# Kernel tuning notes

Hardware: AMD Instinct MI355X
Metric: run time of the kernel (lower is better)

The kernel has to match this reference:

```python
import jax, jax.numpy as jnp
import numpy as np

T, B, X, H, Y, D = 512, 64, 64, 1024, 64, 2


def setup_inputs() -> dict:
    key = jax.random.key(0)
    ks = jax.random.split(key, 13)
    s = 0.02  # weight init scale
    return {
        "x": jax.random.normal(ks[0], (T, B, X), dtype=jnp.float32),
        "enc_w": jax.random.normal(ks[1], (H, X), dtype=jnp.float32) * s,
        "enc_b": jax.random.normal(ks[2], (H,), dtype=jnp.float32) * s,
        "w_ih": jax.random.normal(ks[3], (D, 3 * H, H), dtype=jnp.float32) * s,
        "w_hh": jax.random.normal(ks[4], (D, 3 * H, H), dtype=jnp.float32) * s,
        "b_ih": jax.random.normal(ks[5], (D, 3 * H), dtype=jnp.float32) * s,
        "b_hh": jax.random.normal(ks[6], (D, 3 * H), dtype=jnp.float32) * s,
        "dec_w": jax.random.normal(ks[7], (H, H), dtype=jnp.float32) * s,
        "dec_b": jax.random.normal(ks[8], (H,), dtype=jnp.float32) * s,
        "exp_w": jax.random.normal(ks[9], (Y, H), dtype=jnp.float32) * s,
        "exp_b": jax.random.normal(ks[10], (Y,), dtype=jnp.float32) * s,
        "log_w": jax.random.normal(ks[11], (Y, H), dtype=jnp.float32) * s,
        "log_b": jax.random.normal(ks[12], (Y,), dtype=jnp.float32) * s,
    }


def _gru_cell(x, h, wih, whh, bih, bhh):
    # PyTorch GRUCell semantics
    gi = x @ wih.T + bih  # [B, 3H]
    gh = h @ whh.T + bhh  # [B, 3H]
    i_r, i_z, i_n = jnp.split(gi, 3, axis=-1)
    h_r, h_z, h_n = jnp.split(gh, 3, axis=-1)
    r = jax.nn.sigmoid(i_r + h_r)
    z = jax.nn.sigmoid(i_z + h_z)
    n = jnp.tanh(i_n + r * h_n)
    return (1.0 - z) * n + z * h


def reference(x, enc_w, enc_b, w_ih, w_hh, b_ih, b_hh, dec_w, dec_b,
              exp_w, exp_b, log_w, log_b):
    depth = w_ih.shape[0]
    batch = x.shape[1]
    h0 = jnp.zeros((depth, batch, w_hh.shape[-1]), dtype=x.dtype)

    def step(h_states, x_t):
        rnn_in = jnp.tanh(x_t @ enc_w.T + enc_b)  # encoder
        new_h = []
        for i in range(depth):  # small fixed stack of structurally distinct cells
            h = _gru_cell(rnn_in, h_states[i], w_ih[i], w_hh[i], b_ih[i], b_hh[i])
            new_h.append(h)
            rnn_in = h
        rnn_out = jnp.tanh(rnn_in @ dec_w.T + dec_b)  # decoder
        mean = rnn_out @ exp_w.T + exp_b
        var = jnp.exp(rnn_out @ log_w.T + log_b)
        return jnp.stack(new_h), (mean, var)

    _, (time_mean, time_var) = jax.lax.scan(step, h0, x)
    return time_mean, time_var  # each [T, B, Y]
```

## Files before the change

### kernel.cpp

```cpp
#include <hip/hip_runtime.h>
#include <hip/hip_bf16.h>
#include <cstdint>

#define T_STEPS 512
#define BATCH   64
#define XDIM    64
#define HDIM    1024
#define YDIM    64
#define BH      (BATCH * HDIM)
#define RING_D  32

#define WBLK_BYTES   98304
#define COMBO_BYTES  24576
#define TL1_OFF      16384

typedef unsigned short ushort_t;
typedef uint32_t u32;
typedef unsigned long long u64;
typedef __attribute__((ext_vector_type(8))) short short8;
typedef __attribute__((ext_vector_type(4))) float f32x4;

union U4S8 { uint4 u; short8 s; };

__device__ __forceinline__ u32 f2bf_u(float x) {
  u32 u = __float_as_uint(x);
  return (u + 0x7fffu + ((u >> 16) & 1u)) >> 16;
}
__device__ __forceinline__ ushort_t f2bf(float x) { return (ushort_t)f2bf_u(x); }

__device__ __forceinline__ float sigm(float x) { return 1.0f / (1.0f + expf(-x)); }

__device__ __forceinline__ void st_sc32(u32* p, u32 v) {
  __hip_atomic_store(p, v, __ATOMIC_RELAXED, __HIP_MEMORY_SCOPE_AGENT);
}

__device__ __forceinline__ uint4 ld_g128(const ushort_t* p) {
  uint4 r;
  asm volatile("global_load_dwordx4 %0, %1, off" : "=v"(r) : "v"(p));
  return r;
}

__device__ __forceinline__ int flags_ok(const u32* p, u32 tag) {
  uint4 f;
  asm volatile("global_load_dwordx4 %0, %1, off sc1\n\ts_waitcnt vmcnt(0)"
               : "=v"(f) : "v"(p) : "memory");
  return (f.x >= tag) && (f.y >= tag) && (f.z >= tag) && (f.w >= tag);
}
__device__ __forceinline__ void poll4(const u32* flags, int t, u32 tag) {
  const u32* p = flags + 4 * t;
  while (!flags_ok(p, tag)) __builtin_amdgcn_s_sleep(1);
}

__global__ __launch_bounds__(256) void enc_kernel(
    const float* __restrict__ x, const float* __restrict__ enc_w,
    const float* __restrict__ enc_b, ushort_t* __restrict__ enc_out)
{
  __shared__ float wlds[64 * 65];
  const int lane = threadIdx.x & 63;
  const int wv   = threadIdx.x >> 6;
  const int cb = blockIdx.x & 15;
  const int rb = blockIdx.x >> 4;
  const int j  = cb * 64 + lane;
  const int r0 = rb * 16 + wv * 4;

  const float* wsrc = enc_w + (size_t)cb * 64 * XDIM;
  for (int i = threadIdx.x; i < 4096; i += 256)
    wlds[(i >> 6) * 65 + (i & 63)] = wsrc[i];
  __syncthreads();

  const float* xr = x + (size_t)r0 * XDIM;
  float acc[4] = {0.f, 0.f, 0.f, 0.f};
#pragma unroll
  for (int k = 0; k < XDIM; k += 4) {
    const float w0 = wlds[lane * 65 + k];
    const float w1 = wlds[lane * 65 + k + 1];
    const float w2 = wlds[lane * 65 + k + 2];
    const float w3 = wlds[lane * 65 + k + 3];
#pragma unroll
    for (int rr = 0; rr < 4; ++rr) {
      const float* xp = xr + rr * XDIM + k;
      acc[rr] = fmaf(xp[3], w3, fmaf(xp[2], w2, fmaf(xp[1], w1, fmaf(xp[0], w0, acc[rr]))));
    }
  }
  const float b = enc_b[j];
#pragma unroll
  for (int rr = 0; rr < 4; ++rr)
    enc_out[(size_t)(r0 + rr) * HDIM + j] = f2bf(tanhf(acc[rr] + b));
}

__global__ __launch_bounds__(256) void wprep_kernel(
    const float* __restrict__ w_ih, const float* __restrict__ w_hh,
    ushort_t* __restrict__ wfrag)
{
  const int lane = threadIdx.x & 63;
  const int wv   = threadIdx.x >> 6;
  const int c    = blockIdx.x * 4 + wv;
  const int ko = c & 15;
  const int tl = (c >> 4) & 1;
  const int c2 = (c >> 5) & 3;
  const int bid = c >> 7;
  const int g = c2 >> 1, kh = c2 & 1;
  const int layer = bid >> 7;
  const int j0 = (bid & 127) * 8;
  const float* wsrc = (g ? w_hh : w_ih) + (size_t)layer * 3 * HDIM * HDIM;

  if (tl == 0) {
    const int col = lane & 15, kgrp = lane >> 4;
    const int k = kh * 512 + ko * 32 + kgrp * 8;
    const int row = (col < 8) ? (j0 + col) : (HDIM + j0 + col - 8);
    const float* src = wsrc + (size_t)row * HDIM + k;
    short8 v;
#pragma unroll
    for (int e = 0; e < 8; ++e) v[e] = (short)f2bf(src[e]);
    const size_t byte = (size_t)bid * WBLK_BYTES + c2 * COMBO_BYTES + ko * 1024 + lane * 16;
    *(short8*)((char*)wfrag + byte) = v;
  } else if (lane < 32) {
    const int kgrp = lane >> 3, col = lane & 7;
    const int k = kh * 512 + ko * 32 + kgrp * 8;
    const int row = 2 * HDIM + j0 + col;
    const float* src = wsrc + (size_t)row * HDIM + k;
    short8 v;
#pragma unroll
    for (int e = 0; e < 8; ++e) v[e] = (short)f2bf(src[e]);
    const size_t byte = (size_t)bid * WBLK_BYTES + c2 * COMBO_BYTES + TL1_OFF + ko * 512 + lane * 16;
    *(short8*)((char*)wfrag + byte) = v;
  }
}

__global__ __launch_bounds__(256) void wprep2_kernel(
    const float* __restrict__ dec_w, const float* __restrict__ exp_w,
    const float* __restrict__ log_w,
    ushort_t* __restrict__ dwfrag, ushort_t* __restrict__ hwfrag)
{
  const int lane = threadIdx.x & 63;
  const int wv   = threadIdx.x >> 6;
  const int c    = blockIdx.x * 4 + wv;
  short8 v;
  if (c < 2048) {
    const int nt = c >> 5, kc = c & 31;
    const int row = nt * 16 + (lane & 15);
    const int k   = kc * 32 + (lane >> 4) * 8;
    const float* src = dec_w + (size_t)row * HDIM + k;
#pragma unroll
    for (int e = 0; e < 8; ++e) v[e] = (short)f2bf(src[e]);
    *(short8*)(dwfrag + (size_t)c * 512 + lane * 8) = v;
  } else {
    const int c2 = c - 2048;
    const int nt = c2 >> 5, kc = c2 & 31;
    const int row = nt * 16 + (lane & 15);
    const int k   = kc * 32 + (lane >> 4) * 8;
    const float* src = (row < 64) ? (exp_w + (size_t)row * HDIM + k)
                                  : (log_w + (size_t)(row - 64) * HDIM + k);
#pragma unroll
    for (int e = 0; e < 8; ++e) v[e] = (short)f2bf(src[e]);
    *(short8*)(hwfrag + (size_t)c2 * 512 + lane * 8) = v;
  }
}

__global__ __launch_bounds__(512, 1) void rnn_persist(
    const ushort_t* __restrict__ ench1,
    const ushort_t* __restrict__ wfrag,
    const float* __restrict__ b_ih, const float* __restrict__ b_hh,
    ushort_t* __restrict__ h0ring,
    ushort_t* __restrict__ h1ring,
    ushort_t* __restrict__ h1_all,
    u32* __restrict__ l0_flags, u32* __restrict__ l1_flags)
{
  extern __shared__ char smem[];
  float* lds_part = (float*)(smem + WBLK_BYTES);

  const int tid  = threadIdx.x;
  const int lane = tid & 63;
  const int wid  = tid >> 6;
  const int bid  = blockIdx.x;
  const int layer = bid >> 7;
  const int j0    = (bid & 127) * 8;
  const int mp = wid & 1, g = (wid >> 1) & 1, kh = wid >> 2;
  const int col = lane & 15, kgrp = lane >> 4;
  const bool isL1 = (layer == 1);
  const int gbid = bid & 127;
  u32* ownf = isL1 ? l1_flags : l0_flags;

  {
    const uint4* src = (const uint4*)((const char*)wfrag + (size_t)bid * WBLK_BYTES);
    uint4* dst = (uint4*)smem;
#pragma unroll 4
    for (int i = tid; i < WBLK_BYTES / 16; i += 512) dst[i] = src[i];
  }

  const int c2 = g * 2 + kh;
  const char* w0 = smem + c2 * COMBO_BYTES + lane * 16;
  const char* w1 = smem + c2 * COMBO_BYTES + TL1_OFF + (kgrp * 8 + (col & 7)) * 16;

  float bA = 0.f, bB = 0.f, bC = 0.f;
  {
    const float* bi = b_ih + layer * 3 * HDIM;
    const float* bh = b_hh + layer * 3 * HDIM;
    if (col < 8) {
      const int j = j0 + col;
      bA = bi[j] + bh[j];
      bB = bi[2 * HDIM + j];
      bC = bh[2 * HDIM + j];
    } else {
      const int j = j0 + col - 8;
      bA = bi[HDIM + j] + bh[HDIM + j];
    }
  }

  f32x4 hp = {0.f, 0.f, 0.f, 0.f};

  __syncthreads();

  for (int i = 0; i < T_STEPS; ++i) {
    if (isL1) {
      if (tid < 32) poll4(l0_flags, tid, (u32)(i + 1));
      __syncthreads();
    }

    const ushort_t* A1 = isL1 ? (h0ring + (size_t)(i & (RING_D - 1)) * BH)
                              : (ench1 + (size_t)i * BH);
    const ushort_t* A2 = isL1 ? (h1ring + (size_t)((i - 1) & (RING_D - 1)) * BH)
                              : (h0ring + (size_t)((i - 1) & (RING_D - 1)) * BH);
    const ushort_t* A = g ? A2 : A1;
    const ushort_t* Arow0 = A + (size_t)(mp * 32 + col) * HDIM + kh * 512 + kgrp * 8;
    const ushort_t* Arow1 = Arow0 + 16 * HDIM;

    uint4 areg[32];
    if (g == 0) {
#pragma unroll
      for (int ko = 0; ko < 16; ++ko) {
        areg[2 * ko]     = ld_g128(Arow0 + ko * 32);
        areg[2 * ko + 1] = ld_g128(Arow1 + ko * 32);
      }
    }

    if (tid < 32) {
      poll4(ownf, tid, (u32)i);
      if (!isL1 && i >= RING_D) poll4(l1_flags, tid, (u32)(i - RING_D + 1));
    }
    __syncthreads();

    if (g == 1) {
#pragma unroll
      for (int ko = 0; ko < 16; ++ko) {
        areg[2 * ko]     = ld_g128(Arow0 + ko * 32);
        areg[2 * ko + 1] = ld_g128(Arow1 + ko * 32);
      }
    }

    f32x4 acc00 = {0,0,0,0}, acc01 = {0,0,0,0}, acc10 = {0,0,0,0}, acc11 = {0,0,0,0};
    asm volatile("s_waitcnt vmcnt(16)" ::: "memory");
    __builtin_amdgcn_sched_barrier(0);
#pragma unroll
    for (int ko = 0; ko < 8; ++ko) {
      const short8 b0 = *(const short8*)(w0 + ko * 1024);
      const short8 b1 = *(const short8*)(w1 + ko * 512);
      U4S8 a0, a1; a0.u = areg[2 * ko]; a1.u = areg[2 * ko + 1];
      acc00 = __builtin_amdgcn_mfma_f32_16x16x32_bf16(a0.s, b0, acc00, 0, 0, 0);
      acc01 = __builtin_amdgcn_mfma_f32_16x16x32_bf16(a0.s, b1, acc01, 0, 0, 0);
      acc10 = __builtin_amdgcn_mfma_f32_16x16x32_bf16(a1.s, b0, acc10, 0, 0, 0);
      acc11 = __builtin_amdgcn_mfma_f32_16x16x32_bf16(a1.s, b1, acc11, 0, 0, 0);
    }
    asm volatile("s_waitcnt vmcnt(0)" ::: "memory");
    __builtin_amdgcn_sched_barrier(0);
#pragma unroll
    for (int ko = 8; ko < 16; ++ko) {
      const short8 b0 = *(const short8*)(w0 + ko * 1024);
      const short8 b1 = *(const short8*)(w1 + ko * 512);
      U4S8 a0, a1; a0.u = areg[2 * ko]; a1.u = areg[2 * ko + 1];
      acc00 = __builtin_amdgcn_mfma_f32_16x16x32_bf16(a0.s, b0, acc00, 0, 0, 0);
      acc01 = __builtin_amdgcn_mfma_f32_16x16x32_bf16(a0.s, b1, acc01, 0, 0, 0);
      acc10 = __builtin_amdgcn_mfma_f32_16x16x32_bf16(a1.s, b0, acc10, 0, 0, 0);
      acc11 = __builtin_amdgcn_mfma_f32_16x16x32_bf16(a1.s, b1, acc11, 0, 0, 0);
    }

    const int base = (wid * 4) * 256 + lane * 4;
    *(f32x4*)&lds_part[base      ] = acc00;
    *(f32x4*)&lds_part[base + 256] = acc01;
    *(f32x4*)&lds_part[base + 512] = acc10;
    *(f32x4*)&lds_part[base + 768] = acc11;

    __syncthreads();

    if (wid < 4) {
      const int m = wid, mpe = m >> 1, ime = m & 1;
      const int i00 = ((0 * 4 + 0 * 2 + mpe) * 4 + ime * 2);
      const int i01 = ((1 * 4 + 0 * 2 + mpe) * 4 + ime * 2);
      const int i10 = ((0 * 4 + 1 * 2 + mpe) * 4 + ime * 2);
      const int i11 = ((1 * 4 + 1 * 2 + mpe) * 4 + ime * 2);
      const int lo = lane * 4;
      f32x4 girz = *(f32x4*)&lds_part[i00 * 256 + lo] + *(f32x4*)&lds_part[i01 * 256 + lo];
      f32x4 gin  = *(f32x4*)&lds_part[(i00 + 1) * 256 + lo] + *(f32x4*)&lds_part[(i01 + 1) * 256 + lo];
      f32x4 ghrz = *(f32x4*)&lds_part[i10 * 256 + lo] + *(f32x4*)&lds_part[i11 * 256 + lo];
      f32x4 ghn  = *(f32x4*)&lds_part[(i10 + 1) * 256 + lo] + *(f32x4*)&lds_part[(i11 + 1) * 256 + lo];

      ushort_t* hdst = isL1 ? (h1ring + (size_t)(i & (RING_D - 1)) * BH)
                            : (h0ring + (size_t)(i & (RING_D - 1)) * BH);
      ushort_t* hall = isL1 ? (h1_all + (size_t)i * BH) : (ushort_t*)0;

#pragma unroll
      for (int e = 0; e < 4; ++e) {
        const float rz = sigm(girz[e] + ghrz[e] + bA);
        const float nv = tanhf(gin[e] + bB + rz * (ghn[e] + bC));
        const float zv = __shfl_xor(rz, 8);
        const int b = m * 16 + kgrp * 4 + e;
        float h = 0.f;
        if (col < 8) {
          h = (1.f - zv) * nv + zv * hp[e];
          hp[e] = h;
        }
        const u32 hb = f2bf_u(h);
        const u32 pb = (u32)__shfl_xor((int)hb, 1);
        if (col < 8 && (col & 1) == 0) {
          const u32 pack = hb | (pb << 16);
          st_sc32((u32*)(hdst + b * HDIM + j0 + col), pack);
          if (hall) st_sc32((u32*)(hall + b * HDIM + j0 + col), pack);
        }
      }
    }

    __syncthreads();
    if (tid == 0) st_sc32(ownf + gbid, (u32)(i + 1));
  }
}

#define AST 1032
__global__ __launch_bounds__(512, 1) void dechead_kernel(
    const ushort_t* __restrict__ h1_all,
    const ushort_t* __restrict__ dwfrag, const ushort_t* __restrict__ hwfrag,
    const float* __restrict__ dec_b, const float* __restrict__ exp_b,
    const float* __restrict__ log_b, float* __restrict__ out)
{
  extern __shared__ char smem2[];
  ushort_t* Alds = (ushort_t*)smem2;
  ushort_t* Rlds = Alds + 32 * AST;

  const int tid  = threadIdx.x;
  const int lane = tid & 63;
  const int wv   = tid >> 6;
  const int base = blockIdx.x * 32;

  {
    const uint4* src = (const uint4*)(h1_all + (size_t)base * HDIM);
#pragma unroll
    for (int ii = 0; ii < 8; ++ii) {
      const int idx = ii * 512 + tid;
      const int row = idx >> 7;
      const int k   = (idx & 127) * 8;
      *(uint4*)(Alds + row * AST + k) = src[idx];
    }
  }
  __syncthreads();

  f32x4 acc[8][2];
#pragma unroll
  for (int t = 0; t < 8; ++t) { acc[t][0] = (f32x4){0,0,0,0}; acc[t][1] = (f32x4){0,0,0,0}; }

  const int r0 = lane & 15, kg = lane >> 4;
  const int nt0 = wv * 8;
#pragma unroll 1
  for (int t = 0; t < 8; ++t) {
    const ushort_t* bsrc = dwfrag + (size_t)(nt0 + t) * 32 * 512 + lane * 8;
    f32x4 c0 = acc[t][0], c1 = acc[t][1];
#pragma unroll
    for (int kc = 0; kc < 32; ++kc) {
      const short8 b  = *(const short8*)(bsrc + kc * 512);
      const short8 a0 = *(const short8*)(Alds + r0 * AST + kc * 32 + kg * 8);
      const short8 a1 = *(const short8*)(Alds + (16 + r0) * AST + kc * 32 + kg * 8);
      c0 = __builtin_amdgcn_mfma_f32_16x16x32_bf16(a0, b, c0, 0, 0, 0);
      c1 = __builtin_amdgcn_mfma_f32_16x16x32_bf16(a1, b, c1, 0, 0, 0);
    }
    acc[t][0] = c0; acc[t][1] = c1;
  }

#pragma unroll
  for (int t = 0; t < 8; ++t) {
    const int colc = (nt0 + t) * 16 + r0;
    const float db = dec_b[colc];
#pragma unroll
    for (int m = 0; m < 2; ++m) {
      const f32x4 v = acc[t][m];
#pragma unroll
      for (int e = 0; e < 4; ++e) {
        const int row = m * 16 + kg * 4 + e;
        Rlds[row * AST + colc] = (ushort_t)f2bf_u(tanhf(v[e] + db));
      }
    }
  }
  __syncthreads();

  f32x4 h0a = {0,0,0,0}, h1a = {0,0,0,0};
  {
    const ushort_t* bsrc = hwfrag + (size_t)wv * 32 * 512 + lane * 8;
#pragma unroll
    for (int kc = 0; kc < 32; ++kc) {
      const short8 b  = *(const short8*)(bsrc + kc * 512);
      const short8 a0 = *(const short8*)(Rlds + r0 * AST + kc * 32 + kg * 8);
      const short8 a1 = *(const short8*)(Rlds + (16 + r0) * AST + kc * 32 + kg * 8);
      h0a = __builtin_amdgcn_mfma_f32_16x16x32_bf16(a0, b, h0a, 0, 0, 0);
      h1a = __builtin_amdgcn_mfma_f32_16x16x32_bf16(a1, b, h1a, 0, 0, 0);
    }
  }
  const int y = wv * 16 + r0;
  if (wv < 4) {
    const float eb = exp_b[y];
#pragma unroll
    for (int m = 0; m < 2; ++m) {
      const f32x4 v = (m == 0) ? h0a : h1a;
#pragma unroll
      for (int e = 0; e < 4; ++e) {
        const int row = m * 16 + kg * 4 + e;
        out[(size_t)(base + row) * YDIM + y] = v[e] + eb;
      }
    }
  } else {
    const int yv = y - 64;
    const float lb = log_b[yv];
#pragma unroll
    for (int m = 0; m < 2; ++m) {
      const f32x4 v = (m == 0) ? h0a : h1a;
#pragma unroll
      for (int e = 0; e < 4; ++e) {
        const int row = m * 16 + kg * 4 + e;
        out[(size_t)(T_STEPS * BATCH * YDIM) + (size_t)(base + row) * YDIM + yv] = expf(v[e] + lb);
      }
    }
  }
}

extern "C" void kernel_launch(void* const* d_in, const int* in_sizes, int n_in,
                              void* d_out, int out_size, void* d_ws, size_t ws_size,
                              hipStream_t stream) {
  (void)in_sizes; (void)n_in; (void)out_size; (void)ws_size;
  const float* x     = (const float*)d_in[0];
  const float* enc_w = (const float*)d_in[1];
  const float* enc_b = (const float*)d_in[2];
  const float* w_ih  = (const float*)d_in[3];
  const float* w_hh  = (const float*)d_in[4];
  const float* b_ih  = (const float*)d_in[5];
  const float* b_hh  = (const float*)d_in[6];
  const float* dec_w = (const float*)d_in[7];
  const float* dec_b = (const float*)d_in[8];
  const float* exp_w = (const float*)d_in[9];
  const float* exp_b = (const float*)d_in[10];
  const float* log_w = (const float*)d_in[11];
  const float* log_b = (const float*)d_in[12];
  float* out = (float*)d_out;

  char* ws = (char*)d_ws;
  u32*      l0f     = (u32*)ws;
  u32*      l1f     = (u32*)(ws + 4096);
  ushort_t* wfrag   = (ushort_t*)(ws + 2097152);
  ushort_t* h0ring  = (ushort_t*)(ws + 27262976);
  ushort_t* h1ring  = (ushort_t*)(ws + 31457280);
  ushort_t* ench1   = (ushort_t*)(ws + 35651584);
  ushort_t* dwfrag  = (ushort_t*)(ws + 102760448);
  ushort_t* hwfrag  = (ushort_t*)(ws + 104857600);

  hipMemsetAsync(ws, 0, 8192, stream);
  hipMemsetAsync(ws + 27262976, 0, 8388608, stream);

  enc_kernel<<<32768, 256, 0, stream>>>(x, enc_w, enc_b, ench1);
  wprep_kernel<<<8192, 256, 0, stream>>>(w_ih, w_hh, wfrag);
  wprep2_kernel<<<576, 256, 0, stream>>>(dec_w, exp_w, log_w, dwfrag, hwfrag);

  {
    static int lds_opted = 0;
    if (!lds_opted) {
      hipFuncSetAttribute((const void*)rnn_persist,
                          hipFuncAttributeMaxDynamicSharedMemorySize, 131072);
      hipFuncSetAttribute((const void*)dechead_kernel,
                          hipFuncAttributeMaxDynamicSharedMemorySize, 2 * 32 * AST * 2);
      lds_opted = 1;
    }
    void* args[9];
    args[0] = (void*)&ench1;
    args[1] = (void*)&wfrag;
    args[2] = (void*)&b_ih;
    args[3] = (void*)&b_hh;
    args[4] = (void*)&h0ring;
    args[5] = (void*)&h1ring;
    args[6] = (void*)&ench1;
    args[7] = (void*)&l0f;
    args[8] = (void*)&l1f;
    hipLaunchCooperativeKernel((const void*)rnn_persist, dim3(256), dim3(512),
                               args, 131072, stream);
  }

  dechead_kernel<<<1024, 512, 2 * 32 * AST * 2, stream>>>(
      ench1, dwfrag, hwfrag, dec_b, exp_b, log_b, out);
}
```

Baseline: 5.573 ms.

## Per-wave flag polling on padded flags and coalesced 128-bit hidden-state stores

Replaces the block-wide poll-then-__syncthreads handshake with per-lane polling: each wave spins on its own dependency flags, which are now padded to one per 64-byte line. This lets waves start their global loads independently instead of waiting on a block barrier. Hidden-state outputs are staged in LDS and written as 128-bit row stores instead of scattered 32-bit atomic stores. The trade-off is many more lanes polling global memory each step and a slightly larger LDS footprint.

```diff
diff --git a/kernel.cpp b/kernel.cpp
--- a/kernel.cpp
+++ b/kernel.cpp
@@ -13,6 +13,7 @@
 #define WBLK_BYTES   98304
 #define COMBO_BYTES  24576
 #define TL1_OFF      16384
+#define LDS_TOTAL    (WBLK_BYTES + 32768 + 1024)
 
 typedef unsigned short ushort_t;
 typedef uint32_t u32;
@@ -33,22 +34,21 @@
 __device__ __forceinline__ void st_sc32(u32* p, u32 v) {
   __hip_atomic_store(p, v, __ATOMIC_RELAXED, __HIP_MEMORY_SCOPE_AGENT);
 }
-
+__device__ __forceinline__ void poll_lane(const u32* flags, int idx, u32 tag) {
+  const u32* p = flags + (size_t)idx * 16;
+  while (__hip_atomic_load((u32*)p, __ATOMIC_RELAXED, __HIP_MEMORY_SCOPE_AGENT) < tag)
+    __builtin_amdgcn_s_sleep(1);
+}
 __device__ __forceinline__ uint4 ld_g128(const ushort_t* p) {
   uint4 r;
   asm volatile("global_load_dwordx4 %0, %1, off" : "=v"(r) : "v"(p));
   return r;
 }
-
-__device__ __forceinline__ int flags_ok(const u32* p, u32 tag) {
-  uint4 f;
-  asm volatile("global_load_dwordx4 %0, %1, off sc1\n\ts_waitcnt vmcnt(0)"
-               : "=v"(f) : "v"(p) : "memory");
-  return (f.x >= tag) && (f.y >= tag) && (f.z >= tag) && (f.w >= tag);
-}
-__device__ __forceinline__ void poll4(const u32* flags, int t, u32 tag) {
-  const u32* p = flags + 4 * t;
-  while (!flags_ok(p, tag)) __builtin_amdgcn_s_sleep(1);
+__device__ __forceinline__ void st_sc128(ushort_t* p, uint4 v) {
+  const u64 lo = ((u64)v.y << 32) | (u64)v.x;
+  const u64 hi = ((u64)v.w << 32) | (u64)v.z;
+  __hip_atomic_store((u64*)p,     lo, __ATOMIC_RELAXED, __HIP_MEMORY_SCOPE_AGENT);
+  __hip_atomic_store((u64*)p + 1, hi, __ATOMIC_RELAXED, __HIP_MEMORY_SCOPE_AGENT);
 }
 
 __global__ __launch_bounds__(256) void enc_kernel(
@@ -168,6 +168,7 @@
 {
   extern __shared__ char smem[];
   float* lds_part = (float*)(smem + WBLK_BYTES);
+  u32*   gbuf     = (u32*)(smem + WBLK_BYTES + 32768);
 
   const int tid  = threadIdx.x;
   const int lane = tid & 63;
@@ -180,6 +181,7 @@
   const bool isL1 = (layer == 1);
   const int gbid = bid & 127;
   u32* ownf = isL1 ? l1_flags : l0_flags;
+  const int fidx = kh * 64 + lane;
 
   {
     const uint4* src = (const uint4*)((const char*)wfrag + (size_t)bid * WBLK_BYTES);
@@ -212,9 +214,11 @@
   __syncthreads();
 
   for (int i = 0; i < T_STEPS; ++i) {
-    if (isL1) {
-      if (tid < 32) poll4(l0_flags, tid, (u32)(i + 1));
-      __syncthreads();
+    if (g == 0) {
+      if (isL1) poll_lane(l0_flags, fidx, (u32)(i + 1));
+      else if (i >= RING_D) poll_lane(l1_flags, fidx, (u32)(i - RING_D + 1));
+    } else {
+      poll_lane(ownf, fidx, (u32)i);
     }
 
     const ushort_t* A1 = isL1 ? (h0ring + (size_t)(i & (RING_D - 1)) * BH)
@@ -226,26 +230,10 @@
     const ushort_t* Arow1 = Arow0 + 16 * HDIM;
 
     uint4 areg[32];
-    if (g == 0) {
-#pragma unroll
-      for (int ko = 0; ko < 16; ++ko) {
-        areg[2 * ko]     = ld_g128(Arow0 + ko * 32);
-        areg[2 * ko + 1] = ld_g128(Arow1 + ko * 32);
-      }
-    }
-
-    if (tid < 32) {
-      poll4(ownf, tid, (u32)i);
-      if (!isL1 && i >= RING_D) poll4(l1_flags, tid, (u32)(i - RING_D + 1));
-    }
-    __syncthreads();
-
-    if (g == 1) {
-#pragma unroll
-      for (int ko = 0; ko < 16; ++ko) {
-        areg[2 * ko]     = ld_g128(Arow0 + ko * 32);
-        areg[2 * ko + 1] = ld_g128(Arow1 + ko * 32);
-      }
+#pragma unroll
+    for (int ko = 0; ko < 16; ++ko) {
+      areg[2 * ko]     = ld_g128(Arow0 + ko * 32);
+      areg[2 * ko + 1] = ld_g128(Arow1 + ko * 32);
     }
 
     f32x4 acc00 = {0,0,0,0}, acc01 = {0,0,0,0}, acc10 = {0,0,0,0}, acc11 = {0,0,0,0};
@@ -294,16 +282,11 @@
       f32x4 ghrz = *(f32x4*)&lds_part[i10 * 256 + lo] + *(f32x4*)&lds_part[i11 * 256 + lo];
       f32x4 ghn  = *(f32x4*)&lds_part[(i10 + 1) * 256 + lo] + *(f32x4*)&lds_part[(i11 + 1) * 256 + lo];
 
-      ushort_t* hdst = isL1 ? (h1ring + (size_t)(i & (RING_D - 1)) * BH)
-                            : (h0ring + (size_t)(i & (RING_D - 1)) * BH);
-      ushort_t* hall = isL1 ? (h1_all + (size_t)i * BH) : (ushort_t*)0;
-
 #pragma unroll
       for (int e = 0; e < 4; ++e) {
         const float rz = sigm(girz[e] + ghrz[e] + bA);
         const float nv = tanhf(gin[e] + bB + rz * (ghn[e] + bC));
         const float zv = __shfl_xor(rz, 8);
-        const int b = m * 16 + kgrp * 4 + e;
         float h = 0.f;
         if (col < 8) {
           h = (1.f - zv) * nv + zv * hp[e];
@@ -312,15 +295,28 @@
         const u32 hb = f2bf_u(h);
         const u32 pb = (u32)__shfl_xor((int)hb, 1);
         if (col < 8 && (col & 1) == 0) {
-          const u32 pack = hb | (pb << 16);
-          st_sc32((u32*)(hdst + b * HDIM + j0 + col), pack);
-          if (hall) st_sc32((u32*)(hall + b * HDIM + j0 + col), pack);
+          gbuf[m * 64 + (kgrp * 4 + e) * 4 + (col >> 1)] = hb | (pb << 16);
         }
       }
+
+      asm volatile("s_waitcnt lgkmcnt(0)" ::: "memory");
+      __builtin_amdgcn_sched_barrier(0);
+      if (lane < 16) {
+        uint4 v = *(uint4*)&gbuf[m * 64 + lane * 4];
+        const int row = m * 16 + lane;
+        ushort_t* d0 = (isL1 ? (h1ring + (size_t)(i & (RING_D - 1)) * BH)
+                             : (h0ring + (size_t)(i & (RING_D - 1)) * BH))
+                       + (size_t)row * HDIM + j0;
+        st_sc128(d0, v);
+        if (isL1) {
+          ushort_t* d1 = h1_all + (size_t)i * BH + (size_t)row * HDIM + j0;
+          st_sc128(d1, v);
+        }
+      }
     }
 
     __syncthreads();
-    if (tid == 0) st_sc32(ownf + gbid, (u32)(i + 1));
+    if (tid == 0) st_sc32(ownf + (size_t)gbid * 16, (u32)(i + 1));
   }
 }
 
@@ -449,7 +445,7 @@
 
   char* ws = (char*)d_ws;
   u32*      l0f     = (u32*)ws;
-  u32*      l1f     = (u32*)(ws + 4096);
+  u32*      l1f     = (u32*)(ws + 8192);
   ushort_t* wfrag   = (ushort_t*)(ws + 2097152);
   ushort_t* h0ring  = (ushort_t*)(ws + 27262976);
   ushort_t* h1ring  = (ushort_t*)(ws + 31457280);
@@ -457,7 +453,7 @@
   ushort_t* dwfrag  = (ushort_t*)(ws + 102760448);
   ushort_t* hwfrag  = (ushort_t*)(ws + 104857600);
 
-  hipMemsetAsync(ws, 0, 8192, stream);
+  hipMemsetAsync(ws, 0, 16384, stream);
   hipMemsetAsync(ws + 27262976, 0, 8388608, stream);
 
   enc_kernel<<<32768, 256, 0, stream>>>(x, enc_w, enc_b, ench1);
@@ -467,9 +463,9 @@
   {
     static int lds_opted = 0;
     if (!lds_opted) {
-      hipFuncSetAttribute((const void*)rnn_persist,
-                          hipFuncAttributeMaxDynamicSharedMemorySize, 131072);
-      hipFuncSetAttribute((const void*)dechead_kernel,
+      (void)hipFuncSetAttribute((const void*)rnn_persist,
+                          hipFuncAttributeMaxDynamicSharedMemorySize, LDS_TOTAL);
+      (void)hipFuncSetAttribute((const void*)dechead_kernel,
                           hipFuncAttributeMaxDynamicSharedMemorySize, 2 * 32 * AST * 2);
       lds_opted = 1;
     }
@@ -483,8 +479,8 @@
     args[6] = (void*)&ench1;
     args[7] = (void*)&l0f;
     args[8] = (void*)&l1f;
-    hipLaunchCooperativeKernel((const void*)rnn_persist, dim3(256), dim3(512),
-                               args, 131072, stream);
+    (void)hipLaunchCooperativeKernel((const void*)rnn_persist, dim3(256), dim3(512),
+                               args, LDS_TOTAL, stream);
   }
 
   dechead_kernel<<<1024, 512, 2 * 32 * AST * 2, stream>>>(
```

After: 6.165 ms. +10.6%, slower.

## Double waves per persistent GRU block, one 16-row M tile per wave

Applied to the files above, without the earlier changes.

The persistent recurrent kernel now runs 1024 threads (16 waves) per block instead of 512. Each wave computes a single 16-row batch tile instead of two, which halves per-wave A-operand loads and MFMA chains and shortens the serial per-step critical path. The cost is more waves contending at the per-step barriers, more LDS partial-sum traffic, and register pressure limited by 1024-thread launch bounds. A fallback to a normal launch is added in case the cooperative launch fails.

```diff
diff --git a/kernel.cpp b/kernel.cpp
--- a/kernel.cpp
+++ b/kernel.cpp
@@ -13,6 +13,7 @@
 #define WBLK_BYTES   98304
 #define COMBO_BYTES  24576
 #define TL1_OFF      16384
+#define LDS_TOTAL    131072
 
 typedef unsigned short ushort_t;
 typedef uint32_t u32;
@@ -33,13 +34,11 @@
 __device__ __forceinline__ void st_sc32(u32* p, u32 v) {
   __hip_atomic_store(p, v, __ATOMIC_RELAXED, __HIP_MEMORY_SCOPE_AGENT);
 }
-
 __device__ __forceinline__ uint4 ld_g128(const ushort_t* p) {
   uint4 r;
   asm volatile("global_load_dwordx4 %0, %1, off" : "=v"(r) : "v"(p));
   return r;
 }
-
 __device__ __forceinline__ int flags_ok(const u32* p, u32 tag) {
   uint4 f;
   asm volatile("global_load_dwordx4 %0, %1, off sc1\n\ts_waitcnt vmcnt(0)"
@@ -157,7 +156,7 @@
   }
 }
 
-__global__ __launch_bounds__(512, 1) void rnn_persist(
+__global__ __launch_bounds__(1024, 1) void rnn_persist(
     const ushort_t* __restrict__ ench1,
     const ushort_t* __restrict__ wfrag,
     const float* __restrict__ b_ih, const float* __restrict__ b_hh,
@@ -175,7 +174,7 @@
   const int bid  = blockIdx.x;
   const int layer = bid >> 7;
   const int j0    = (bid & 127) * 8;
-  const int mp = wid & 1, g = (wid >> 1) & 1, kh = wid >> 2;
+  const int mq = wid & 3, g = (wid >> 2) & 1, kh = wid >> 3;
   const int col = lane & 15, kgrp = lane >> 4;
   const bool isL1 = (layer == 1);
   const int gbid = bid & 127;
@@ -184,8 +183,8 @@
   {
     const uint4* src = (const uint4*)((const char*)wfrag + (size_t)bid * WBLK_BYTES);
     uint4* dst = (uint4*)smem;
-#pragma unroll 4
-    for (int i = tid; i < WBLK_BYTES / 16; i += 512) dst[i] = src[i];
+#pragma unroll 2
+    for (int i = tid; i < WBLK_BYTES / 16; i += 1024) dst[i] = src[i];
   }
 
   const int c2 = g * 2 + kh;
@@ -222,16 +221,12 @@
     const ushort_t* A2 = isL1 ? (h1ring + (size_t)((i - 1) & (RING_D - 1)) * BH)
                               : (h0ring + (size_t)((i - 1) & (RING_D - 1)) * BH);
     const ushort_t* A = g ? A2 : A1;
-    const ushort_t* Arow0 = A + (size_t)(mp * 32 + col) * HDIM + kh * 512 + kgrp * 8;
-    const ushort_t* Arow1 = Arow0 + 16 * HDIM;
-
-    uint4 areg[32];
+    const ushort_t* Arow = A + (size_t)(mq * 16 + col) * HDIM + kh * 512 + kgrp * 8;
+
+    uint4 areg[16];
     if (g == 0) {
 #pragma unroll
-      for (int ko = 0; ko < 16; ++ko) {
-        areg[2 * ko]     = ld_g128(Arow0 + ko * 32);
-        areg[2 * ko + 1] = ld_g128(Arow1 + ko * 32);
-      }
+      for (int ko = 0; ko < 16; ++ko) areg[ko] = ld_g128(Arow + ko * 32);
     }
 
     if (tid < 32) {
@@ -242,24 +237,19 @@
 
     if (g == 1) {
 #pragma unroll
-      for (int ko = 0; ko < 16; ++ko) {
-        areg[2 * ko]     = ld_g128(Arow0 + ko * 32);
-        areg[2 * ko + 1] = ld_g128(Arow1 + ko * 32);
-      }
-    }
-
-    f32x4 acc00 = {0,0,0,0}, acc01 = {0,0,0,0}, acc10 = {0,0,0,0}, acc11 = {0,0,0,0};
-    asm volatile("s_waitcnt vmcnt(16)" ::: "memory");
+      for (int ko = 0; ko < 16; ++ko) areg[ko] = ld_g128(Arow + ko * 32);
+    }
+
+    f32x4 acc0 = {0,0,0,0}, acc1 = {0,0,0,0};
+    asm volatile("s_waitcnt vmcnt(8)" ::: "memory");
     __builtin_amdgcn_sched_barrier(0);
 #pragma unroll
     for (int ko = 0; ko < 8; ++ko) {
       const short8 b0 = *(const short8*)(w0 + ko * 1024);
       const short8 b1 = *(const short8*)(w1 + ko * 512);
-      U4S8 a0, a1; a0.u = areg[2 * ko]; a1.u = areg[2 * ko + 1];
-      acc00 = __builtin_amdgcn_mfma_f32_16x16x32_bf16(a0.s, b0, acc00, 0, 0, 0);
-      acc01 = __builtin_amdgcn_mfma_f32_16x16x32_bf16(a0.s, b1, acc01, 0, 0, 0);
-      acc10 = __builtin_amdgcn_mfma_f32_16x16x32_bf16(a1.s, b0, acc10, 0, 0, 0);
-      acc11 = __builtin_amdgcn_mfma_f32_16x16x32_bf16(a1.s, b1, acc11, 0, 0, 0);
+      U4S8 a; a.u = areg[ko];
+      acc0 = __builtin_amdgcn_mfma_f32_16x16x32_bf16(a.s, b0, acc0, 0, 0, 0);
+      acc1 = __builtin_amdgcn_mfma_f32_16x16x32_bf16(a.s, b1, acc1, 0, 0, 0);
     }
     asm volatile("s_waitcnt vmcnt(0)" ::: "memory");
     __builtin_amdgcn_sched_barrier(0);
@@ -267,32 +257,28 @@
     for (int ko = 8; ko < 16; ++ko) {
       const short8 b0 = *(const short8*)(w0 + ko * 1024);
       const short8 b1 = *(const short8*)(w1 + ko * 512);
-      U4S8 a0, a1; a0.u = areg[2 * ko]; a1.u = areg[2 * ko + 1];
-      acc00 = __builtin_amdgcn_mfma_f32_16x16x32_bf16(a0.s, b0, acc00, 0, 0, 0);
-      acc01 = __builtin_amdgcn_mfma_f32_16x16x32_bf16(a0.s, b1, acc01, 0, 0, 0);
-      acc10 = __builtin_amdgcn_mfma_f32_16x16x32_bf16(a1.s, b0, acc10, 0, 0, 0);
-      acc11 = __builtin_amdgcn_mfma_f32_16x16x32_bf16(a1.s, b1, acc11, 0, 0, 0);
-    }
-
-    const int base = (wid * 4) * 256 + lane * 4;
-    *(f32x4*)&lds_part[base      ] = acc00;
-    *(f32x4*)&lds_part[base + 256] = acc01;
-    *(f32x4*)&lds_part[base + 512] = acc10;
-    *(f32x4*)&lds_part[base + 768] = acc11;
+      U4S8 a; a.u = areg[ko];
+      acc0 = __builtin_amdgcn_mfma_f32_16x16x32_bf16(a.s, b0, acc0, 0, 0, 0);
+      acc1 = __builtin_amdgcn_mfma_f32_16x16x32_bf16(a.s, b1, acc1, 0, 0, 0);
+    }
+
+    const int base = (wid * 2) * 256 + lane * 4;
+    *(f32x4*)&lds_part[base      ] = acc0;
+    *(f32x4*)&lds_part[base + 256] = acc1;
 
     __syncthreads();
 
     if (wid < 4) {
-      const int m = wid, mpe = m >> 1, ime = m & 1;
-      const int i00 = ((0 * 4 + 0 * 2 + mpe) * 4 + ime * 2);
-      const int i01 = ((1 * 4 + 0 * 2 + mpe) * 4 + ime * 2);
-      const int i10 = ((0 * 4 + 1 * 2 + mpe) * 4 + ime * 2);
-      const int i11 = ((1 * 4 + 1 * 2 + mpe) * 4 + ime * 2);
+      const int m = wid;
       const int lo = lane * 4;
-      f32x4 girz = *(f32x4*)&lds_part[i00 * 256 + lo] + *(f32x4*)&lds_part[i01 * 256 + lo];
-      f32x4 gin  = *(f32x4*)&lds_part[(i00 + 1) * 256 + lo] + *(f32x4*)&lds_part[(i01 + 1) * 256 + lo];
-      f32x4 ghrz = *(f32x4*)&lds_part[i10 * 256 + lo] + *(f32x4*)&lds_part[i11 * 256 + lo];
-      f32x4 ghn  = *(f32x4*)&lds_part[(i10 + 1) * 256 + lo] + *(f32x4*)&lds_part[(i11 + 1) * 256 + lo];
+      const int t_ih0 = (0 * 8 + 0 * 4 + m) * 2;
+      const int t_hh0 = (0 * 8 + 1 * 4 + m) * 2;
+      const int t_ih1 = (1 * 8 + 0 * 4 + m) * 2;
+      const int t_hh1 = (1 * 8 + 1 * 4 + m) * 2;
+      f32x4 girz = *(f32x4*)&lds_part[t_ih0 * 256 + lo] + *(f32x4*)&lds_part[t_ih1 * 256 + lo];
+      f32x4 gin  = *(f32x4*)&lds_part[(t_ih0 + 1) * 256 + lo] + *(f32x4*)&lds_part[(t_ih1 + 1) * 256 + lo];
+      f32x4 ghrz = *(f32x4*)&lds_part[t_hh0 * 256 + lo] + *(f32x4*)&lds_part[t_hh1 * 256 + lo];
+      f32x4 ghn  = *(f32x4*)&lds_part[(t_hh0 + 1) * 256 + lo] + *(f32x4*)&lds_part[(t_hh1 + 1) * 256 + lo];
 
       ushort_t* hdst = isL1 ? (h1ring + (size_t)(i & (RING_D - 1)) * BH)
                             : (h0ring + (size_t)(i & (RING_D - 1)) * BH);
@@ -465,14 +451,10 @@
   wprep2_kernel<<<576, 256, 0, stream>>>(dec_w, exp_w, log_w, dwfrag, hwfrag);
 
   {
-    static int lds_opted = 0;
-    if (!lds_opted) {
-      hipFuncSetAttribute((const void*)rnn_persist,
-                          hipFuncAttributeMaxDynamicSharedMemorySize, 131072);
-      hipFuncSetAttribute((const void*)dechead_kernel,
-                          hipFuncAttributeMaxDynamicSharedMemorySize, 2 * 32 * AST * 2);
-      lds_opted = 1;
-    }
+    (void)hipFuncSetAttribute((const void*)rnn_persist,
+                        hipFuncAttributeMaxDynamicSharedMemorySize, LDS_TOTAL);
+    (void)hipFuncSetAttribute((const void*)dechead_kernel,
+                        hipFuncAttributeMaxDynamicSharedMemorySize, 2 * 32 * AST * 2);
     void* args[9];
     args[0] = (void*)&ench1;
     args[1] = (void*)&wfrag;
@@ -483,8 +465,13 @@
     args[6] = (void*)&ench1;
     args[7] = (void*)&l0f;
     args[8] = (void*)&l1f;
-    hipLaunchCooperativeKernel((const void*)rnn_persist, dim3(256), dim3(512),
-                               args, 131072, stream);
+    hipError_t cerr = hipLaunchCooperativeKernel((const void*)rnn_persist,
+                                                 dim3(256), dim3(1024),
+                                                 args, LDS_TOTAL, stream);
+    if (cerr != hipSuccess) {
+      rnn_persist<<<256, 1024, LDS_TOTAL, stream>>>(
+          ench1, wfrag, b_ih, b_hh, h0ring, h1ring, ench1, l0f, l1f);
+    }
   }
 
   dechead_kernel<<<1024, 512, 2 * 32 * AST * 2, stream>>>(
```

New measurement: 6.651 ms. 1.19x slower.
